# Performance work log

Hardware: AMD Instinct MI355X
Metric: run time of the kernel (lower is better)

The kernel has to match this reference:

```python
import jax, jax.numpy as jnp
import numpy as np

K = 3
IN_C, OUT_C = 64, 64
B, N, E = 2, 50000, 800000


def setup_inputs() -> dict:
    key = jax.random.key(0)
    k1, k2, k3, k4, k5 = jax.random.split(key, 5)
    x = jax.random.normal(k1, (B, N, IN_C), dtype=jnp.float32)
    edge_index = jax.random.randint(k2, (2, E), 0, N, dtype=jnp.int64)
    edge_weight = jax.random.uniform(k3, (E,), dtype=jnp.float32)
    stdv = 1.0 / np.sqrt(IN_C * K)
    weight = jax.random.uniform(k4, (K, IN_C, OUT_C), dtype=jnp.float32, minval=-stdv, maxval=stdv)
    bias = jax.random.uniform(k5, (OUT_C,), dtype=jnp.float32, minval=-stdv, maxval=stdv)
    return {"x": x, "edge_index": edge_index, "edge_weight": edge_weight, "weight": weight, "bias": bias}


def reference(x, edge_index, edge_weight, weight, bias):
    row, col = edge_index[0], edge_index[1]
    num_nodes = x.shape[1]
    # remove self loops (mask them out; equivalent math)
    keep = (row != col)
    ew = jnp.where(keep, edge_weight, 0.0)
    # degree counts edges per source node (ones), excluding self loops
    deg = jax.ops.segment_sum(keep.astype(x.dtype), row, num_segments=num_nodes)
    deg_inv_sqrt = jnp.where(deg > 0, deg ** -0.5, 0.0)
    lap = -deg_inv_sqrt[row] * ew * deg_inv_sqrt[col]  # [E]

    def spmm(m):
        # m: [B, N, C] -> gather cols, scale by lap, scatter-add to rows
        vals = m[:, col, :] * lap[None, :, None]        # [B, E, C]
        return jnp.zeros_like(m).at[:, row, :].add(vals)

    Tx0 = x
    out = jnp.matmul(Tx0, weight[0])
    Tx1 = spmm(Tx0)
    out = out + jnp.matmul(Tx1, weight[1])
    for k in range(2, weight.shape[0]):
        Tx2 = 2.0 * spmm(Tx1) - Tx0
        out = out + jnp.matmul(Tx2, weight[k])
        Tx0, Tx1 = Tx1, Tx2
    return out + bias
```

## Files before the change

### kernel.cpp

```cpp
#include <hip/hip_runtime.h>

#define N_NODES 50000
#define N_EDGES 800000
#define N_B 2
#define N_C 64
#define BN_ROWS (N_B * N_NODES)

typedef __attribute__((ext_vector_type(8))) short short8;
typedef __attribute__((ext_vector_type(4))) float f32x4;

__device__ inline unsigned short f2bf(float f) {
  unsigned int u = __float_as_uint(f);
  return (unsigned short)((u + 0x7fffu + ((u >> 16) & 1u)) >> 16);
}
__device__ inline float bf2f(unsigned short h) { return __uint_as_float(((unsigned int)h) << 16); }
__device__ inline float lof(unsigned int u) { return __uint_as_float(u << 16); }
__device__ inline float hif(unsigned int u) { return __uint_as_float(u & 0xffff0000u); }

__global__ __launch_bounds__(256) void k_deg(const int* __restrict__ ei, int* __restrict__ deg) {
  int e = blockIdx.x * 256 + threadIdx.x;
  if (e >= N_EDGES) return;
  int r = ei[e];
  int c = ei[N_EDGES + e];
  if (r != c) atomicAdd(&deg[r], 1);
}

__global__ __launch_bounds__(256) void k_offsets(const int* __restrict__ deg, int* __restrict__ counter,
                                                 int* __restrict__ rowptr, int* __restrict__ cursor,
                                                 float* __restrict__ dis) {
  int n = blockIdx.x * 256 + threadIdx.x;
  int lane = threadIdx.x & 63;
  int d = (n < N_NODES) ? deg[n] : 0;
  int pre = d;
#pragma unroll
  for (int off = 1; off < 64; off <<= 1) {
    int v = __shfl_up(pre, off);
    if (lane >= off) pre += v;
  }
  int waveTotal = __shfl(pre, 63);
  int wbase = 0;
  if (lane == 63) wbase = atomicAdd(counter, waveTotal);
  wbase = __shfl(wbase, 63);
  if (n < N_NODES) {
    int off0 = wbase + pre - d;
    rowptr[n] = off0;
    cursor[n] = off0;
    dis[n] = d > 0 ? rsqrtf((float)d) : 0.0f;
  }
}

__global__ __launch_bounds__(256) void k_fill(const int* __restrict__ ei, const float* __restrict__ ew,
                                              const float* __restrict__ dis, int* __restrict__ cursor,
                                              int2* __restrict__ ccv) {
  int e = blockIdx.x * 256 + threadIdx.x;
  if (e >= N_EDGES) return;
  int r = ei[e];
  int c = ei[N_EDGES + e];
  if (r == c) return;
  float v = -dis[r] * ew[e] * dis[c];
  int pos = atomicAdd(&cursor[r], 1);
  ccv[pos] = make_int2(c, __float_as_int(v));
}

__global__ __launch_bounds__(256) void k_cvt(const float* __restrict__ x, unsigned short* __restrict__ xb) {
  int i = blockIdx.x * 256 + threadIdx.x;
  if (i >= BN_ROWS * 16) return;
  float4 v = ((const float4*)x)[i];
  ushort4 h;
  h.x = f2bf(v.x); h.y = f2bf(v.y); h.z = f2bf(v.z); h.w = f2bf(v.w);
  ((ushort4*)xb)[i] = h;
}

#define UNPK_FMA(Q, A0, A1, A2, A3, A4, A5, A6, A7, V) \
  A0 += (V) * lof(Q.x); A1 += (V) * hif(Q.x); \
  A2 += (V) * lof(Q.y); A3 += (V) * hif(Q.y); \
  A4 += (V) * lof(Q.z); A5 += (V) * hif(Q.z); \
  A6 += (V) * lof(Q.w); A7 += (V) * hif(Q.w);

#define RED3(A) { A += __shfl_xor(A, 8); A += __shfl_xor(A, 16); A += __shfl_xor(A, 32); }

template <int BFOUT>
__global__ __launch_bounds__(256) void k_spmm(const unsigned short* __restrict__ src, void* __restrict__ dstv,
                                              const int* __restrict__ rowptr, const int* __restrict__ deg,
                                              const int2* __restrict__ ccv) {
  int n = (blockIdx.x * 256 + threadIdx.x) >> 6;
  int lane = threadIdx.x & 63;
  if (n >= N_NODES) return;
  const int g = lane >> 3;
  const int cg = lane & 7;
  const unsigned short* s0 = src;
  const unsigned short* s1 = src + (size_t)N_NODES * N_C;
  int r0 = rowptr[n];
  int end = r0 + deg[n];
  float a00 = 0, a01 = 0, a02 = 0, a03 = 0, a04 = 0, a05 = 0, a06 = 0, a07 = 0;
  float a10 = 0, a11 = 0, a12 = 0, a13 = 0, a14 = 0, a15 = 0, a16 = 0, a17 = 0;
#pragma unroll 2
  for (int i = r0; i < end; i += 8) {
    int idx = i + g;
    bool ok = idx < end;
    int2 pe = ccv[ok ? idx : (end - 1)];
    float val = ok ? __int_as_float(pe.y) : 0.0f;
    size_t off = (size_t)pe.x * N_C + cg * 8;
    uint4 q0 = *(const uint4*)(s0 + off);
    uint4 q1 = *(const uint4*)(s1 + off);
    UNPK_FMA(q0, a00, a01, a02, a03, a04, a05, a06, a07, val)
    UNPK_FMA(q1, a10, a11, a12, a13, a14, a15, a16, a17, val)
  }
  RED3(a00) RED3(a01) RED3(a02) RED3(a03) RED3(a04) RED3(a05) RED3(a06) RED3(a07)
  RED3(a10) RED3(a11) RED3(a12) RED3(a13) RED3(a14) RED3(a15) RED3(a16) RED3(a17)
  if (BFOUT) {
    unsigned short* d = (unsigned short*)dstv;
    if (g == 0) {
      uint4 o;
      o.x = (unsigned)f2bf(a00) | ((unsigned)f2bf(a01) << 16);
      o.y = (unsigned)f2bf(a02) | ((unsigned)f2bf(a03) << 16);
      o.z = (unsigned)f2bf(a04) | ((unsigned)f2bf(a05) << 16);
      o.w = (unsigned)f2bf(a06) | ((unsigned)f2bf(a07) << 16);
      *(uint4*)(d + (size_t)n * N_C + cg * 8) = o;
    } else if (g == 1) {
      uint4 o;
      o.x = (unsigned)f2bf(a10) | ((unsigned)f2bf(a11) << 16);
      o.y = (unsigned)f2bf(a12) | ((unsigned)f2bf(a13) << 16);
      o.z = (unsigned)f2bf(a14) | ((unsigned)f2bf(a15) << 16);
      o.w = (unsigned)f2bf(a16) | ((unsigned)f2bf(a17) << 16);
      *(uint4*)(d + ((size_t)N_NODES + n) * N_C + cg * 8) = o;
    }
  } else {
    float* d = (float*)dstv;
    if (g == 0) {
      *(float4*)(d + (size_t)n * N_C + cg * 8) = make_float4(a00, a01, a02, a03);
      *(float4*)(d + (size_t)n * N_C + cg * 8 + 4) = make_float4(a04, a05, a06, a07);
    } else if (g == 1) {
      *(float4*)(d + ((size_t)N_NODES + n) * N_C + cg * 8) = make_float4(a10, a11, a12, a13);
      *(float4*)(d + ((size_t)N_NODES + n) * N_C + cg * 8 + 4) = make_float4(a14, a15, a16, a17);
    }
  }
}

__global__ __launch_bounds__(256) void k_gemm(const unsigned short* __restrict__ xb,
                                              const unsigned short* __restrict__ t1h,
                                              const float* __restrict__ w,
                                              const float* __restrict__ bias,
                                              float* out) {
  __shared__ unsigned short bp[6 * 4 * 64 * 8];
  const int t = threadIdx.x;
  for (int idx = t; idx < 1536; idx += 256) {
    int kt = idx >> 8;
    int rem = idx & 255;
    int c = rem >> 6;
    int l = rem & 63;
    int ch = kt >> 1;
    int kbase = (kt & 1) * 32 + (l >> 4) * 8;
    int n = c * 16 + (l & 15);
    unsigned short* dst = &bp[idx * 8];
#pragma unroll
    for (int j = 0; j < 8; ++j) {
      int k = kbase + j;
      float v;
      if (ch == 0)      v = w[k * 64 + n] - w[8192 + k * 64 + n];
      else if (ch == 1) v = w[4096 + k * 64 + n];
      else              v = 2.0f * w[8192 + k * 64 + n];
      dst[j] = f2bf(v);
    }
  }
  __syncthreads();

  const int wid = t >> 6;
  const int lane = t & 63;
  const size_t base = (size_t)blockIdx.x * 64 + (size_t)wid * 16;
  const int arow = lane & 15;
  const int ko = (lane >> 4) * 8;
  size_t row = base + arow;
  if (row > (size_t)(BN_ROWS - 1)) row = BN_ROWS - 1;

  const unsigned short* xp = xb + row * 64 + ko;
  const unsigned short* tp = t1h + row * 64 + ko;
  const float* zp = out + row * 64 + ko;
  short8 ax0 = *(const short8*)(xp);
  short8 ax1 = *(const short8*)(xp + 32);
  short8 at0 = *(const short8*)(tp);
  short8 at1 = *(const short8*)(tp + 32);
  float4 z00 = *(const float4*)(zp);
  float4 z01 = *(const float4*)(zp + 4);
  float4 z10 = *(const float4*)(zp + 32);
  float4 z11 = *(const float4*)(zp + 36);
  short8 az0, az1;
  az0[0] = (short)f2bf(z00.x); az0[1] = (short)f2bf(z00.y);
  az0[2] = (short)f2bf(z00.z); az0[3] = (short)f2bf(z00.w);
  az0[4] = (short)f2bf(z01.x); az0[5] = (short)f2bf(z01.y);
  az0[6] = (short)f2bf(z01.z); az0[7] = (short)f2bf(z01.w);
  az1[0] = (short)f2bf(z10.x); az1[1] = (short)f2bf(z10.y);
  az1[2] = (short)f2bf(z10.z); az1[3] = (short)f2bf(z10.w);
  az1[4] = (short)f2bf(z11.x); az1[5] = (short)f2bf(z11.y);
  az1[6] = (short)f2bf(z11.z); az1[7] = (short)f2bf(z11.w);

  const int col = lane & 15;
  const int rgrp = lane >> 4;

#pragma unroll
  for (int c = 0; c < 4; ++c) {
    const unsigned short* bb = &bp[(size_t)c * 64 * 8];
    short8 b0 = *(const short8*)(bb + (0 * 4 * 64 + lane) * 8);
    short8 b1 = *(const short8*)(bb + (1 * 4 * 64 + lane) * 8);
    short8 b2 = *(const short8*)(bb + (2 * 4 * 64 + lane) * 8);
    short8 b3 = *(const short8*)(bb + (3 * 4 * 64 + lane) * 8);
    short8 b4 = *(const short8*)(bb + (4 * 4 * 64 + lane) * 8);
    short8 b5 = *(const short8*)(bb + (5 * 4 * 64 + lane) * 8);
    f32x4 acc = {0.f, 0.f, 0.f, 0.f};
    acc = __builtin_amdgcn_mfma_f32_16x16x32_bf16(ax0, b0, acc, 0, 0, 0);
    acc = __builtin_amdgcn_mfma_f32_16x16x32_bf16(ax1, b1, acc, 0, 0, 0);
    acc = __builtin_amdgcn_mfma_f32_16x16x32_bf16(at0, b2, acc, 0, 0, 0);
    acc = __builtin_amdgcn_mfma_f32_16x16x32_bf16(at1, b3, acc, 0, 0, 0);
    acc = __builtin_amdgcn_mfma_f32_16x16x32_bf16(az0, b4, acc, 0, 0, 0);
    acc = __builtin_amdgcn_mfma_f32_16x16x32_bf16(az1, b5, acc, 0, 0, 0);
    const float bcol = bias[c * 16 + col];
#pragma unroll
    for (int j = 0; j < 4; ++j) {
      size_t r = base + (size_t)(rgrp * 4 + j);
      if (r < BN_ROWS) out[r * 64 + c * 16 + col] = acc[j] + bcol;
    }
  }
}

extern "C" void kernel_launch(void* const* d_in, const int* in_sizes, int n_in,
                              void* d_out, int out_size, void* d_ws, size_t ws_size,
                              hipStream_t stream) {
  const float* x = (const float*)d_in[0];
  const int* ei = (const int*)d_in[1];
  const float* ew = (const float*)d_in[2];
  const float* w = (const float*)d_in[3];
  const float* bias = (const float*)d_in[4];
  float* out = (float*)d_out;

  int* ws32 = (int*)d_ws;
  const size_t NA = 50048;
  int* deg = ws32;
  int* counter = deg + N_NODES;
  int* cursor = ws32 + NA;
  float* dis = (float*)(cursor + NA);
  int* rowptr = (int*)(dis + NA);
  int2* ccv = (int2*)(rowptr + NA);
  unsigned short* xb = (unsigned short*)(rowptr + NA + 2 * N_EDGES);
  unsigned short* t1h = xb + (size_t)BN_ROWS * N_C;
  const size_t NEED = ((size_t)(4 * NA + 2 * N_EDGES) + (size_t)BN_ROWS * N_C) * 4;
  if (ws_size < NEED) return;

  hipMemsetAsync(deg, 0, (N_NODES + 1) * sizeof(int), stream);
  k_cvt<<<(BN_ROWS * 16 + 255) / 256, 256, 0, stream>>>(x, xb);
  k_deg<<<(N_EDGES + 255) / 256, 256, 0, stream>>>(ei, deg);
  k_offsets<<<(N_NODES + 255) / 256, 256, 0, stream>>>(deg, counter, rowptr, cursor, dis);
  k_fill<<<(N_EDGES + 255) / 256, 256, 0, stream>>>(ei, ew, dis, cursor, ccv);
  k_spmm<1><<<(N_NODES * 64 + 255) / 256, 256, 0, stream>>>(xb, t1h, rowptr, deg, ccv);
  k_spmm<0><<<(N_NODES * 64 + 255) / 256, 256, 0, stream>>>(t1h, out, rowptr, deg, ccv);
  k_gemm<<<(BN_ROWS + 63) / 64, 256, 0, stream>>>(xb, t1h, w, bias, out);
}
```

Before: 279.3 us.

## Build CSR via two-level bucket partition instead of global atomic fill

Replaces the per-edge global atomic cursor fill with a two-pass scheme. Edges are first partitioned into 256-row buckets through shared-memory staging, then each bucket is scattered into CSR order using shared-memory atomics. A block-level scan now computes rowptr locally. This aims to cut contended global atomics and random 8-byte scatters, at the cost of extra kernel launches and a staging buffer that aliases t1h.

```diff
diff --git a/kernel.cpp b/kernel.cpp
--- a/kernel.cpp
+++ b/kernel.cpp
@@ -5,6 +5,8 @@
 #define N_B 2
 #define N_C 64
 #define BN_ROWS (N_B * N_NODES)
+#define NBKT 196
+#define PCAP 32
 
 typedef __attribute__((ext_vector_type(8))) short short8;
 typedef __attribute__((ext_vector_type(4))) float f32x4;
@@ -25,41 +27,119 @@
   if (r != c) atomicAdd(&deg[r], 1);
 }
 
-__global__ __launch_bounds__(256) void k_offsets(const int* __restrict__ deg, int* __restrict__ counter,
-                                                 int* __restrict__ rowptr, int* __restrict__ cursor,
-                                                 float* __restrict__ dis) {
-  int n = blockIdx.x * 256 + threadIdx.x;
-  int lane = threadIdx.x & 63;
+__global__ __launch_bounds__(256) void k_bsum(const int* __restrict__ deg, float* __restrict__ dis,
+                                              int* __restrict__ bsum) {
+  __shared__ int wsum[4];
+  int t = threadIdx.x;
+  int n = blockIdx.x * 256 + t;
   int d = (n < N_NODES) ? deg[n] : 0;
-  int pre = d;
+  if (n < N_NODES) dis[n] = d > 0 ? rsqrtf((float)d) : 0.0f;
+  int s = d;
 #pragma unroll
-  for (int off = 1; off < 64; off <<= 1) {
-    int v = __shfl_up(pre, off);
-    if (lane >= off) pre += v;
-  }
-  int waveTotal = __shfl(pre, 63);
-  int wbase = 0;
-  if (lane == 63) wbase = atomicAdd(counter, waveTotal);
-  wbase = __shfl(wbase, 63);
-  if (n < N_NODES) {
-    int off0 = wbase + pre - d;
-    rowptr[n] = off0;
-    cursor[n] = off0;
-    dis[n] = d > 0 ? rsqrtf((float)d) : 0.0f;
-  }
-}
-
-__global__ __launch_bounds__(256) void k_fill(const int* __restrict__ ei, const float* __restrict__ ew,
-                                              const float* __restrict__ dis, int* __restrict__ cursor,
-                                              int2* __restrict__ ccv) {
-  int e = blockIdx.x * 256 + threadIdx.x;
-  if (e >= N_EDGES) return;
-  int r = ei[e];
-  int c = ei[N_EDGES + e];
-  if (r == c) return;
-  float v = -dis[r] * ew[e] * dis[c];
-  int pos = atomicAdd(&cursor[r], 1);
-  ccv[pos] = make_int2(c, __float_as_int(v));
+  for (int off = 1; off < 64; off <<= 1) s += __shfl_xor(s, off);
+  if ((t & 63) == 0) wsum[t >> 6] = s;
+  __syncthreads();
+  if (t == 0) bsum[blockIdx.x] = wsum[0] + wsum[1] + wsum[2] + wsum[3];
+}
+
+__global__ __launch_bounds__(256) void k_scanb(const int* __restrict__ bsum, int* __restrict__ stageBase,
+                                               int* __restrict__ stageCur) {
+  __shared__ int sa[256];
+  __shared__ int sb[256];
+  int t = threadIdx.x;
+  int v = (t < NBKT) ? bsum[t] : 0;
+  sa[t] = v;
+  __syncthreads();
+  int* src = sa; int* dst = sb;
+  for (int off = 1; off < 256; off <<= 1) {
+    int x = src[t];
+    if (t >= off) x += src[t - off];
+    dst[t] = x;
+    __syncthreads();
+    int* tmp = src; src = dst; dst = tmp;
+  }
+  int excl = src[t] - v;
+  if (t < NBKT) { stageBase[t] = excl; stageCur[t] = excl; }
+}
+
+__global__ __launch_bounds__(256) void k_part(const int* __restrict__ ei, const float* __restrict__ ew,
+                                              const float* __restrict__ dis, int* __restrict__ stageCur,
+                                              unsigned long long* __restrict__ stage) {
+  __shared__ unsigned long long sbuf[NBKT * PCAP];
+  __shared__ int scnt[NBKT];
+  int t = threadIdx.x;
+  for (int i = t; i < NBKT; i += 256) scnt[i] = 0;
+  __syncthreads();
+  int e0 = blockIdx.x * 4096;
+#pragma unroll 1
+  for (int rnd = 0; rnd < 16; ++rnd) {
+    int e = e0 + rnd * 256 + t;
+    if (e < N_EDGES) {
+      int r = ei[e];
+      int c = ei[N_EDGES + e];
+      if (r != c) {
+        float v = -dis[r] * ew[e] * dis[c];
+        int b = r >> 8;
+        unsigned long long p = ((unsigned long long)__float_as_uint(v) << 32)
+                             | ((unsigned long long)(r & 255) << 16) | (unsigned)c;
+        int pos = atomicAdd(&scnt[b], 1);
+        if (pos < PCAP) {
+          sbuf[b * PCAP + pos] = p;
+        } else {
+          int g = atomicAdd(&stageCur[b], 1);
+          stage[g] = p;
+        }
+      }
+    }
+  }
+  __syncthreads();
+  int wave = t >> 6, lane = t & 63;
+  for (int b = wave; b < NBKT; b += 4) {
+    int nl = scnt[b];
+    if (nl > PCAP) nl = PCAP;
+    if (nl == 0) continue;
+    int gbase;
+    if (lane == 0) gbase = atomicAdd(&stageCur[b], nl);
+    gbase = __shfl(gbase, 0);
+    if (lane < nl) stage[gbase + lane] = sbuf[b * PCAP + lane];
+  }
+}
+
+__global__ __launch_bounds__(256) void k_build(const int* __restrict__ deg, const int* __restrict__ stageBase,
+                                               const unsigned long long* __restrict__ stage,
+                                               int* __restrict__ rowptr, int2* __restrict__ ccv) {
+  __shared__ int sa[256];
+  __shared__ int sb[256];
+  __shared__ int cur[256];
+  __shared__ int shr[2];
+  int t = threadIdx.x;
+  int n = blockIdx.x * 256 + t;
+  int d = (n < N_NODES) ? deg[n] : 0;
+  sa[t] = d;
+  __syncthreads();
+  int* src = sa; int* dst = sb;
+  for (int off = 1; off < 256; off <<= 1) {
+    int x = src[t];
+    if (t >= off) x += src[t - off];
+    dst[t] = x;
+    __syncthreads();
+    int* tmp = src; src = dst; dst = tmp;
+  }
+  int excl = src[t] - d;
+  cur[t] = excl;
+  if (t == 255) shr[0] = src[255];
+  if (t == 0) shr[1] = stageBase[blockIdx.x];
+  __syncthreads();
+  int cnt = shr[0], base = shr[1];
+  if (n < N_NODES) rowptr[n] = base + excl;
+  for (int i = t; i < cnt; i += 256) {
+    unsigned long long p = stage[base + i];
+    int c = (int)(p & 0xFFFFu);
+    int rl = (int)((p >> 16) & 0xFFu);
+    unsigned int vb = (unsigned int)(p >> 32);
+    int pos = atomicAdd(&cur[rl], 1);
+    ccv[base + pos] = make_int2(c, (int)vb);
+  }
 }
 
 __global__ __launch_bounds__(256) void k_cvt(const float* __restrict__ x, unsigned short* __restrict__ xb) {
@@ -235,21 +315,25 @@
   int* ws32 = (int*)d_ws;
   const size_t NA = 50048;
   int* deg = ws32;
-  int* counter = deg + N_NODES;
-  int* cursor = ws32 + NA;
-  float* dis = (float*)(cursor + NA);
+  int* bsum = ws32 + NA;
+  int* stageBase = bsum + 256;
+  int* stageCur = bsum + 512;
+  float* dis = (float*)(ws32 + 2 * NA);
   int* rowptr = (int*)(dis + NA);
   int2* ccv = (int2*)(rowptr + NA);
   unsigned short* xb = (unsigned short*)(rowptr + NA + 2 * N_EDGES);
   unsigned short* t1h = xb + (size_t)BN_ROWS * N_C;
+  unsigned long long* stage = (unsigned long long*)t1h;
   const size_t NEED = ((size_t)(4 * NA + 2 * N_EDGES) + (size_t)BN_ROWS * N_C) * 4;
   if (ws_size < NEED) return;
 
-  hipMemsetAsync(deg, 0, (N_NODES + 1) * sizeof(int), stream);
+  hipMemsetAsync(deg, 0, N_NODES * sizeof(int), stream);
   k_cvt<<<(BN_ROWS * 16 + 255) / 256, 256, 0, stream>>>(x, xb);
   k_deg<<<(N_EDGES + 255) / 256, 256, 0, stream>>>(ei, deg);
-  k_offsets<<<(N_NODES + 255) / 256, 256, 0, stream>>>(deg, counter, rowptr, cursor, dis);
-  k_fill<<<(N_EDGES + 255) / 256, 256, 0, stream>>>(ei, ew, dis, cursor, ccv);
+  k_bsum<<<NBKT, 256, 0, stream>>>(deg, dis, bsum);
+  k_scanb<<<1, 256, 0, stream>>>(bsum, stageBase, stageCur);
+  k_part<<<NBKT, 256, 0, stream>>>(ei, ew, dis, stageCur, stage);
+  k_build<<<NBKT, 256, 0, stream>>>(deg, stageBase, stage, rowptr, ccv);
   k_spmm<1><<<(N_NODES * 64 + 255) / 256, 256, 0, stream>>>(xb, t1h, rowptr, deg, ccv);
   k_spmm<0><<<(N_NODES * 64 + 255) / 256, 256, 0, stream>>>(t1h, out, rowptr, deg, ccv);
   k_gemm<<<(BN_ROWS + 63) / 64, 256, 0, stream>>>(xb, t1h, w, bias, out);
```

New measurement: 429.4 us. +53.7%, slower.
